# Kernel tuning notes

Hardware: AMD Instinct MI355X
Metric: run time of the kernel (lower is better)

## Reference

```python
import jax, jax.numpy as jnp
import numpy as np

B_GRAPHS, N_NODES = 16, 4096
IN_CH, HID = 256, 512
HEADS, HC = 1, 512  # SGFormerAttention(hidden, heads=1, head_channels=hidden)
NUM_LAYERS = 2
LN_EPS = 1e-5
QK_EPS = 1e-6


def setup_inputs() -> dict:
    key = jax.random.key(0)
    ks = jax.random.split(key, 10)

    def w(k, shape, scale=0.02):
        return jax.random.normal(k, shape, jnp.float32) * scale

    inp = {
        "x": jax.random.normal(ks[0], (B_GRAPHS * N_NODES, IN_CH), jnp.float32),
        "fc0_w": w(ks[1], (HID, IN_CH)),
        "fc0_b": jnp.zeros((HID,), jnp.float32),
        "ln0_g": jnp.ones((HID,), jnp.float32),
        "ln0_b": jnp.zeros((HID,), jnp.float32),
        "q0_w": w(ks[2], (HEADS * HC, HID)),
        "k0_w": w(ks[3], (HEADS * HC, HID)),
        "v0_w": w(ks[4], (HEADS * HC, HID)),
        "ln1_g": jnp.ones((HID,), jnp.float32),
        "ln1_b": jnp.zeros((HID,), jnp.float32),
        "q1_w": w(ks[5], (HEADS * HC, HID)),
        "k1_w": w(ks[6], (HEADS * HC, HID)),
        "v1_w": w(ks[7], (HEADS * HC, HID)),
        "ln2_g": jnp.ones((HID,), jnp.float32),
        "ln2_b": jnp.zeros((HID,), jnp.float32),
        "batch": jnp.repeat(jnp.arange(B_GRAPHS, dtype=jnp.int32), N_NODES),
        "num_graphs": B_GRAPHS,
    }
    return inp


def layernorm(x, g, b):
    mu = x.mean(axis=-1, keepdims=True)
    var = ((x - mu) ** 2).mean(axis=-1, keepdims=True)
    return (x - mu) / jnp.sqrt(var + LN_EPS) * g + b


def sg_attention(x, qw, kw, vw):
    # x: [B, N, HID]; linear (kernelized) global attention, softmax-free.
    B, N, _ = x.shape
    q = (x @ qw.T).reshape(B, N, HEADS, HC)
    k = (x @ kw.T).reshape(B, N, HEADS, HC)
    v = (x @ vw.T).reshape(B, N, HEADS, HC)
    q = jnp.where(q == 0, QK_EPS, q)
    k = jnp.where(k == 0, QK_EPS, k)
    q = q / jnp.linalg.norm(q, axis=-1, keepdims=True)
    k = k / jnp.linalg.norm(k, axis=-1, keepdims=True)
    kvs = jnp.einsum('blhm,blhd->bhmd', k, v)          # [B,H,HC,HC]
    num = jnp.einsum('bnhm,bhmd->bnhd', q, kvs) + N * v
    ks_sum = k.sum(axis=1)                             # [B,H,HC]
    denom = jnp.einsum('bnhm,bhm->bnh', q, ks_sum)[..., None] + float(N)
    return (num / denom).mean(axis=2)                  # [B,N,HC] (mean over heads)


def reference(x, fc0_w, fc0_b, ln0_g, ln0_b,
              q0_w, k0_w, v0_w, ln1_g, ln1_b,
              q1_w, k1_w, v1_w, ln2_g, ln2_b,
              batch, num_graphs):
    total = x.shape[0]
    # stable sort by graph id, remember inverse permutation
    indices = jnp.argsort(batch, stable=True)
    rev_perm = jnp.zeros((total,), jnp.int32).at[indices].set(
        jnp.arange(total, dtype=jnp.int32))
    xs = x[indices]
    # uniform graph sizes -> to_dense_batch is a reshape; mask is all-True
    h = xs.reshape(num_graphs, total // num_graphs, x.shape[1])
    h = h @ fc0_w.T + fc0_b
    h = jax.nn.relu(layernorm(h, ln0_g, ln0_b))  # dropout inactive (eval)
    layers = [h]
    for (qw, kw, vw, g, b) in ((q0_w, k0_w, v0_w, ln1_g, ln1_b),
                               (q1_w, k1_w, v1_w, ln2_g, ln2_b)):
        a = sg_attention(layers[-1], qw, kw, vw)
        a = (a + layers[-1]) / 2.0
        a = jax.nn.relu(layernorm(a, g, b))
        layers.append(a)
    out = layers[-1].reshape(total, -1)
    return out[rev_perm]
```

## Files before the change

### kernel.cpp

```cpp
#include <hip/hip_runtime.h>

#define TNODES 65536
#define NGRAPH 16
#define NNODE  4096
#define INCH   256
#define HID    512

using u16 = unsigned short;
using u32 = unsigned int;
using v8s = __attribute__((ext_vector_type(8))) short;
using v4f = __attribute__((ext_vector_type(4))) float;

__device__ __forceinline__ float bf2f(u16 u) {
    union { u32 i; float f; } v; v.i = ((u32)u) << 16; return v.f;
}
__device__ __forceinline__ u16 f2bf(float f) {
    union { float f; u32 i; } v; v.f = f;
    u32 x = v.i;
    return (u16)((x + 0x7fffu + ((x >> 16) & 1u)) >> 16);
}
__device__ __forceinline__ void up4(uint2 p, float* f) {
    f[0] = __uint_as_float(p.x << 16); f[1] = __uint_as_float(p.x & 0xffff0000u);
    f[2] = __uint_as_float(p.y << 16); f[3] = __uint_as_float(p.y & 0xffff0000u);
}
__device__ __forceinline__ uint2 pk4(float a, float b, float c, float d) {
    uint2 r;
    r.x = (u32)f2bf(a) | ((u32)f2bf(b) << 16);
    r.y = (u32)f2bf(c) | ((u32)f2bf(d) << 16);
    return r;
}

#define MFMA(a, b, c) __builtin_amdgcn_mfma_f32_16x16x32_bf16((a), (b), (c), 0, 0, 0)

#define GLD16(gp, sp) __builtin_amdgcn_global_load_lds( \
    (const __attribute__((address_space(1))) u32*)(const void*)(gp), \
    (__attribute__((address_space(3))) u32*)(void*)(sp), 16, 0, 0)

__global__ void k_cvt4(const float* __restrict__ s, u16* __restrict__ d, int n4) {
    for (int i = blockIdx.x * blockDim.x + threadIdx.x; i < n4; i += gridDim.x * blockDim.x) {
        float4 f = ((const float4*)s)[i];
        ((uint2*)d)[i] = pk4(f.x, f.y, f.z, f.w);
    }
}

__global__ void k_zero(float* __restrict__ p, int n) {
    int i = blockIdx.x * 256 + threadIdx.x;
    if (i < n) p[i] = 0.f;
}

__global__ void k_red4(const u16* __restrict__ p, u16* __restrict__ o, int n8) {
    const size_t P = (size_t)NGRAPH * HID * HID;
    for (int i = blockIdx.x * blockDim.x + threadIdx.x; i < n8; i += gridDim.x * blockDim.x) {
        size_t b = (size_t)i * 8;
        float s[8] = {0.f, 0.f, 0.f, 0.f, 0.f, 0.f, 0.f, 0.f};
        #pragma unroll
        for (int ss = 0; ss < 4; ++ss) {
            v8s v = *(const v8s*)(p + ss * P + b);
            const u16* vp = (const u16*)&v;
            #pragma unroll
            for (int j = 0; j < 8; ++j) s[j] += bf2f(vp[j]);
        }
        uint2 lo = pk4(s[0], s[1], s[2], s[3]);
        uint2 hi = pk4(s[4], s[5], s[6], s[7]);
        uint4 w; w.x = lo.x; w.y = lo.y; w.z = hi.x; w.w = hi.y;
        *(uint4*)(o + b) = w;
    }
}

template<int LDK, int KLEN>
__device__ __forceinline__ void gemm_core(const u16* __restrict__ A,
                                          const u16* __restrict__ W,
                                          u16* sA, u16* sW, v4f (&acc)[8][2]) {
    const int t = threadIdx.x, lane = t & 63;
    const int q = lane >> 4, m15 = lane & 15;
    const int w = t >> 6, wr = w >> 2, wc = w & 3;

    #pragma unroll
    for (int n = 0; n < 8; ++n)
        #pragma unroll
        for (int rt = 0; rt < 2; ++rt)
            #pragma unroll
            for (int e = 0; e < 4; ++e) acc[n][rt][e] = 0.f;

    int aoff[2], woff[8];
    #pragma unroll
    for (int rt = 0; rt < 2; ++rt) {
        int r = wr * 32 + rt * 16 + m15;
        aoff[rt] = r * 32 + ((q ^ ((r >> 1) & 3)) * 8);
    }
    #pragma unroll
    for (int n = 0; n < 8; ++n) {
        int r = wc * 128 + n * 16 + m15;
        woff[n] = r * 32 + ((q ^ ((r >> 1) & 3)) * 8);
    }

    auto stage = [&](int k0, int buf) {
        u16* dW = sW + buf * (512 * 32);
        #pragma unroll
        for (int p = 0; p < 4; ++p) {
            int sf = p * 512 + t, row = sf >> 2, sl = sf & 3;
            int gc = k0 + ((sl ^ ((row >> 1) & 3)) * 8);
            GLD16(W + (size_t)row * LDK + gc, dW + sf * 8);
        }
        if (t < 256) {
            int row = t >> 2, sl = t & 3;
            int gc = k0 + ((sl ^ ((row >> 1) & 3)) * 8);
            GLD16(A + (size_t)row * LDK + gc, sA + buf * (64 * 32) + t * 8);
        }
    };

    stage(0, 0);
    __syncthreads();
    const int KT = KLEN / 32;
    int cur = 0;
    for (int kt = 0; kt < KT; ++kt) {
        if (kt + 1 < KT) stage((kt + 1) * 32, cur ^ 1);
        const u16* cA = sA + cur * (64 * 32);
        const u16* cW = sW + cur * (512 * 32);
        v8s b0 = *(const v8s*)(cA + aoff[0]);
        v8s b1 = *(const v8s*)(cA + aoff[1]);
        #pragma unroll
        for (int n = 0; n < 8; ++n) {
            v8s af = *(const v8s*)(cW + woff[n]);
            acc[n][0] = MFMA(af, b0, acc[n][0]);
            acc[n][1] = MFMA(af, b1, acc[n][1]);
        }
        __syncthreads();
        cur ^= 1;
    }
}


__launch_bounds__(512, 4)
__global__ void k_fc(const u16* __restrict__ xb, const u16* __restrict__ wb,
                     const float* __restrict__ bias, const float* __restrict__ lg,
                     const float* __restrict__ lb, u16* __restrict__ h) {
    __shared__ u16 sA[2][64 * 32];
    __shared__ u16 sW[2][512 * 32];
    __shared__ float red[2][64][4];
    __shared__ float rowv[2][64];
    const int t = threadIdx.x, lane = t & 63, w = t >> 6;
    const int q = lane >> 4, m15 = lane & 15;
    const int wr = w >> 2, wc = w & 3;
    const int bx = (int)blockIdx.x;
    const int swz = (bx & 7) * ((int)gridDim.x >> 3) + (bx >> 3);
    const int r0 = swz * 64;
    v4f acc[8][2];
    gemm_core<INCH, INCH>(xb + (size_t)r0 * INCH, wb, &sA[0][0], &sW[0][0], acc);

    float sm0 = 0.f, sm1 = 0.f, sq0 = 0.f, sq1 = 0.f;
    #pragma unroll
    for (int n = 0; n < 8; ++n) {
        int c = wc * 128 + n * 16 + q * 4;
        float4 bi = *(const float4*)(bias + c);
        const float* bp = &bi.x;
        #pragma unroll
        for (int rt = 0; rt < 2; ++rt)
            #pragma unroll
            for (int e = 0; e < 4; ++e) {
                float a = acc[n][rt][e] + bp[e];
                acc[n][rt][e] = a;
                if (rt == 0) { sm0 += a; sq0 += a * a; } else { sm1 += a; sq1 += a * a; }
            }
    }
    sm0 += __shfl_xor(sm0, 16); sm0 += __shfl_xor(sm0, 32);
    sq0 += __shfl_xor(sq0, 16); sq0 += __shfl_xor(sq0, 32);
    sm1 += __shfl_xor(sm1, 16); sm1 += __shfl_xor(sm1, 32);
    sq1 += __shfl_xor(sq1, 16); sq1 += __shfl_xor(sq1, 32);
    if (lane < 16) {
        red[0][wr * 32 + m15][wc] = sm0; red[0][wr * 32 + 16 + m15][wc] = sm1;
        red[1][wr * 32 + m15][wc] = sq0; red[1][wr * 32 + 16 + m15][wc] = sq1;
    }
    __syncthreads();
    if (t < 64) {
        float tt = red[0][t][0] + red[0][t][1] + red[0][t][2] + red[0][t][3];
        float t2 = red[1][t][0] + red[1][t][1] + red[1][t][2] + red[1][t][3];
        float mu = tt * (1.f / HID);
        float rs = rsqrtf(t2 * (1.f / HID) - mu * mu + 1e-5f);
        rowv[0][t] = mu; rowv[1][t] = rs;
    }
    __syncthreads();
    #pragma unroll
    for (int n = 0; n < 8; ++n) {
        int c = wc * 128 + n * 16 + q * 4;
        float4 g4 = *(const float4*)(lg + c);
        float4 b4 = *(const float4*)(lb + c);
        #pragma unroll
        for (int rt = 0; rt < 2; ++rt) {
            int row = wr * 32 + rt * 16 + m15;
            float mu = rowv[0][row], rs = rowv[1][row];
            float v0 = (acc[n][rt][0] - mu) * rs * g4.x + b4.x;
            float v1 = (acc[n][rt][1] - mu) * rs * g4.y + b4.y;
            float v2 = (acc[n][rt][2] - mu) * rs * g4.z + b4.z;
            float v3 = (acc[n][rt][3] - mu) * rs * g4.w + b4.w;
            v0 = v0 > 0.f ? v0 : 0.f; v1 = v1 > 0.f ? v1 : 0.f;
            v2 = v2 > 0.f ? v2 : 0.f; v3 = v3 > 0.f ? v3 : 0.f;
            *(uint2*)&h[(size_t)(r0 + row) * HID + c] = pk4(v0, v1, v2, v3);
        }
    }
}

__launch_bounds__(512, 4)
__global__ void k_proj(const u16* __restrict__ hsrc, const u16* __restrict__ wkb,
                       const u16* __restrict__ wvb, u16* __restrict__ kt,
                       u16* __restrict__ vt, float* __restrict__ vo,
                       float* __restrict__ ksum) {
    __shared__ char smem[8192 + 65536 + 1024 + 256];
    u16* sA = (u16*)smem;
    u16* sW = (u16*)(smem + 8192);
    u16* sT = sW;
    float (*red)[4] = (float(*)[4])(smem + 8192 + 65536);
    float* rowv = (float*)(smem + 8192 + 65536 + 1024);
    const int t = threadIdx.x, lane = t & 63, w = t >> 6;
    const int q = lane >> 4, m15 = lane & 15;
    const int wr = w >> 2, wc = w & 3;
    const int bx = (int)blockIdx.x;
    const int swz = (bx & 7) * ((int)gridDim.x >> 3) + (bx >> 3);
    const int r0 = swz * 64;
    const int g = swz >> 6;
    const int lbase = (swz & 63) * 64;
    const int mode = blockIdx.y;
    v4f acc[8][2];
    gemm_core<HID, HID>(hsrc + (size_t)r0 * HID, mode ? wvb : wkb,
                        sA, sW, acc);

    if (mode == 0) {
        float sq0 = 0.f, sq1 = 0.f;
        #pragma unroll
        for (int n = 0; n < 8; ++n)
            #pragma unroll
            for (int rt = 0; rt < 2; ++rt)
                #pragma unroll
                for (int e = 0; e < 4; ++e) {
                    float vv = acc[n][rt][e];
                    if (vv == 0.f) vv = 1e-6f;
                    acc[n][rt][e] = vv;
                    if (rt == 0) sq0 += vv * vv; else sq1 += vv * vv;
                }
        sq0 += __shfl_xor(sq0, 16); sq0 += __shfl_xor(sq0, 32);
        sq1 += __shfl_xor(sq1, 16); sq1 += __shfl_xor(sq1, 32);
        if (lane < 16) {
            red[wr * 32 + m15][wc] = sq0; red[wr * 32 + 16 + m15][wc] = sq1;
        }
        __syncthreads();
        if (t < 64)
            rowv[t] = rsqrtf(red[t][0] + red[t][1] + red[t][2] + red[t][3]);
        __syncthreads();
        #pragma unroll
        for (int n = 0; n < 8; ++n)
            #pragma unroll
            for (int rt = 0; rt < 2; ++rt) {
                int row = wr * 32 + rt * 16 + m15;
                float rn = rowv[row];
                #pragma unroll
                for (int e = 0; e < 4; ++e) {
                    int c = wc * 128 + n * 16 + q * 4 + e;
                    sT[(c << 6) + (row ^ ((c & 7) << 3))] = f2bf(acc[n][rt][e] * rn);
                }
            }
        __syncthreads();
        const int ch = t;
        u16* op = kt + ((size_t)(g * 512 + ch)) * NNODE + lbase;
        float sum = 0.f;
        #pragma unroll
        for (int jj = 0; jj < 8; ++jj) {
            v8s cvec = *(const v8s*)&sT[(ch << 6) + jj * 8];
            int l0 = (jj ^ (ch & 7)) * 8;
            *(v8s*)(op + l0) = cvec;
            const u16* cp = (const u16*)&cvec;
            #pragma unroll
            for (int i = 0; i < 8; ++i) sum += bf2f(cp[i]);
        }
        atomicAdd(&ksum[g * 512 + ch], sum);
    } else {
        #pragma unroll
        for (int n = 0; n < 8; ++n) {
            int c = wc * 128 + n * 16 + q * 4;
            #pragma unroll
            for (int rt = 0; rt < 2; ++rt) {
                int row = wr * 32 + rt * 16 + m15;
                float4 o = {acc[n][rt][0], acc[n][rt][1], acc[n][rt][2], acc[n][rt][3]};
                *(float4*)&vo[(size_t)(r0 + row) * HID + c] = o;
                #pragma unroll
                for (int e = 0; e < 4; ++e)
                    sT[((c + e) << 6) + (row ^ (((c + e) & 7) << 3))] = f2bf(acc[n][rt][e]);
            }
        }
        __syncthreads();
        const int ch = t;
        u16* op = vt + ((size_t)(g * 512 + ch)) * NNODE + lbase;
        #pragma unroll
        for (int jj = 0; jj < 8; ++jj) {
            v8s cvec = *(const v8s*)&sT[(ch << 6) + jj * 8];
            int l0 = (jj ^ (ch & 7)) * 8;
            *(v8s*)(op + l0) = cvec;
        }
    }
}

__launch_bounds__(512, 4)
__global__ void k_kvmm2(const u16* __restrict__ kt, const u16* __restrict__ vt,
                        u16* __restrict__ kvp) {
    __shared__ u16 sA[2][64 * 32];
    __shared__ u16 sW[2][512 * 32];
    const int t = threadIdx.x, lane = t & 63, w = t >> 6;
    const int q = lane >> 4, m15 = lane & 15;
    const int wr = w >> 2, wc = w & 3;
    const int bx = (int)blockIdx.x;
    const int swz = (bx & 7) * 64 + (bx >> 3);
    const int db = swz & 7, s = (swz >> 3) & 3, g = swz >> 5;
    const u16* A = vt + ((size_t)(g * 512 + db * 64)) * NNODE + s * 1024;
    const u16* W = kt + ((size_t)(g * 512)) * NNODE + s * 1024;
    v4f acc[8][2];
    gemm_core<NNODE, 1024>(A, W, &sA[0][0], &sW[0][0], acc);
    u16* plane = kvp + (size_t)s * NGRAPH * HID * HID;
    #pragma unroll
    for (int n = 0; n < 8; ++n) {
        int m = wc * 128 + n * 16 + q * 4;
        #pragma unroll
        for (int rt = 0; rt < 2; ++rt) {
            int d = db * 64 + wr * 32 + rt * 16 + m15;
            *(uint2*)&plane[((size_t)(g * 512) + d) * 512 + m] =
                pk4(acc[n][rt][0], acc[n][rt][1], acc[n][rt][2], acc[n][rt][3]);
        }
    }
}

__launch_bounds__(512, 4)
__global__ void k_qnorm(const u16* __restrict__ hsrc, const u16* __restrict__ qwb,
                        const float* __restrict__ ks, u16* __restrict__ qo,
                        float* __restrict__ dnv) {
    __shared__ u16 sA[2][64 * 32];
    __shared__ u16 sW[2][512 * 32];
    __shared__ float red[2][64][4];
    __shared__ float rowv[64];
    const int t = threadIdx.x, lane = t & 63, w = t >> 6;
    const int q = lane >> 4, m15 = lane & 15;
    const int wr = w >> 2, wc = w & 3;
    const int bx = (int)blockIdx.x;
    const int swz = (bx & 7) * ((int)gridDim.x >> 3) + (bx >> 3);
    const int r0 = swz * 64;
    const int gi = swz >> 6;
    v4f acc[8][2];
    gemm_core<HID, HID>(hsrc + (size_t)r0 * HID, qwb, &sA[0][0], &sW[0][0], acc);

    float ss0 = 0.f, ss1 = 0.f, ws0 = 0.f, ws1 = 0.f;
    #pragma unroll
    for (int n = 0; n < 8; ++n) {
        int c = wc * 128 + n * 16 + q * 4;
        float4 kv = *(const float4*)(ks + (gi << 9) + c);
        const float* kp = &kv.x;
        #pragma unroll
        for (int rt = 0; rt < 2; ++rt)
            #pragma unroll
            for (int e = 0; e < 4; ++e) {
                float vv = acc[n][rt][e];
                if (vv == 0.f) vv = 1e-6f;
                acc[n][rt][e] = vv;
                if (rt == 0) { ss0 += vv * vv; ws0 += vv * kp[e]; }
                else         { ss1 += vv * vv; ws1 += vv * kp[e]; }
            }
    }
    ss0 += __shfl_xor(ss0, 16); ss0 += __shfl_xor(ss0, 32);
    ss1 += __shfl_xor(ss1, 16); ss1 += __shfl_xor(ss1, 32);
    ws0 += __shfl_xor(ws0, 16); ws0 += __shfl_xor(ws0, 32);
    ws1 += __shfl_xor(ws1, 16); ws1 += __shfl_xor(ws1, 32);
    if (lane < 16) {
        red[0][wr * 32 + m15][wc] = ss0; red[0][wr * 32 + 16 + m15][wc] = ss1;
        red[1][wr * 32 + m15][wc] = ws0; red[1][wr * 32 + 16 + m15][wc] = ws1;
    }
    __syncthreads();
    if (t < 64) {
        float st = red[0][t][0] + red[0][t][1] + red[0][t][2] + red[0][t][3];
        float wt = red[1][t][0] + red[1][t][1] + red[1][t][2] + red[1][t][3];
        float rn = rsqrtf(st);
        rowv[t] = rn;
        dnv[r0 + t] = 1.f / (rn * wt + (float)NNODE);
    }
    __syncthreads();
    #pragma unroll
    for (int n = 0; n < 8; ++n) {
        int c = wc * 128 + n * 16 + q * 4;
        #pragma unroll
        for (int rt = 0; rt < 2; ++rt) {
            int row = wr * 32 + rt * 16 + m15;
            float rn = rowv[row];
            *(uint2*)&qo[(size_t)(r0 + row) * HID + c] =
                pk4(acc[n][rt][0] * rn, acc[n][rt][1] * rn,
                    acc[n][rt][2] * rn, acc[n][rt][3] * rn);
        }
    }
}

__launch_bounds__(512, 4)
__global__ void k_attn2(const u16* __restrict__ qhat, const u16* __restrict__ kvstb,
                        const float* __restrict__ dnv, const float* __restrict__ vsrc,
                        const u16* __restrict__ hsrc, const float* __restrict__ lg,
                        const float* __restrict__ lb, u16* __restrict__ outb,
                        float* __restrict__ outf) {
    __shared__ u16 sA[2][64 * 32];
    __shared__ u16 sW[2][512 * 32];
    __shared__ float red[2][64][4];
    __shared__ float rowv[2][64];
    const int t = threadIdx.x, lane = t & 63, w = t >> 6;
    const int q = lane >> 4, m15 = lane & 15;
    const int wr = w >> 2, wc = w & 3;
    const int bx = (int)blockIdx.x;
    const int swz = (bx & 7) * ((int)gridDim.x >> 3) + (bx >> 3);
    const int r0 = swz * 64;
    const int gi = swz >> 6;
    v4f acc[8][2];
    gemm_core<HID, HID>(qhat + (size_t)r0 * HID, kvstb + (size_t)gi * HID * HID,
                        &sA[0][0], &sW[0][0], acc);

    const float dv0 = dnv[r0 + wr * 32 + m15];
    const float dv1 = dnv[r0 + wr * 32 + 16 + m15];
    float sm0 = 0.f, sm1 = 0.f, sq0 = 0.f, sq1 = 0.f;
    #pragma unroll
    for (int n = 0; n < 8; ++n) {
        int c = wc * 128 + n * 16 + q * 4;
        #pragma unroll
        for (int rt = 0; rt < 2; ++rt) {
            int row = wr * 32 + rt * 16 + m15;
            size_t og = (size_t)(r0 + row) * HID + c;
            float hh[4]; up4(*(const uint2*)&hsrc[og], hh);
            float4 vv = *(const float4*)&vsrc[og];
            const float* vp = &vv.x;
            float dv = rt ? dv1 : dv0;
            #pragma unroll
            for (int e = 0; e < 4; ++e) {
                float a = ((acc[n][rt][e] + (float)NNODE * vp[e]) * dv + hh[e]) * 0.5f;
                acc[n][rt][e] = a;
                if (rt == 0) { sm0 += a; sq0 += a * a; } else { sm1 += a; sq1 += a * a; }
            }
        }
    }
    sm0 += __shfl_xor(sm0, 16); sm0 += __shfl_xor(sm0, 32);
    sq0 += __shfl_xor(sq0, 16); sq0 += __shfl_xor(sq0, 32);
    sm1 += __shfl_xor(sm1, 16); sm1 += __shfl_xor(sm1, 32);
    sq1 += __shfl_xor(sq1, 16); sq1 += __shfl_xor(sq1, 32);
    if (lane < 16) {
        red[0][wr * 32 + m15][wc] = sm0; red[0][wr * 32 + 16 + m15][wc] = sm1;
        red[1][wr * 32 + m15][wc] = sq0; red[1][wr * 32 + 16 + m15][wc] = sq1;
    }
    __syncthreads();
    if (t < 64) {
        float tt = red[0][t][0] + red[0][t][1] + red[0][t][2] + red[0][t][3];
        float t2 = red[1][t][0] + red[1][t][1] + red[1][t][2] + red[1][t][3];
        float mu = tt * (1.f / HID);
        float rs = rsqrtf(t2 * (1.f / HID) - mu * mu + 1e-5f);
        rowv[0][t] = mu; rowv[1][t] = rs;
    }
    __syncthreads();
    #pragma unroll
    for (int n = 0; n < 8; ++n) {
        int c = wc * 128 + n * 16 + q * 4;
        float4 g4 = *(const float4*)(lg + c);
        float4 b4 = *(const float4*)(lb + c);
        #pragma unroll
        for (int rt = 0; rt < 2; ++rt) {
            int row = wr * 32 + rt * 16 + m15;
            float mu = rowv[0][row], rs = rowv[1][row];
            float v0 = (acc[n][rt][0] - mu) * rs * g4.x + b4.x;
            float v1 = (acc[n][rt][1] - mu) * rs * g4.y + b4.y;
            float v2 = (acc[n][rt][2] - mu) * rs * g4.z + b4.z;
            float v3 = (acc[n][rt][3] - mu) * rs * g4.w + b4.w;
            v0 = v0 > 0.f ? v0 : 0.f; v1 = v1 > 0.f ? v1 : 0.f;
            v2 = v2 > 0.f ? v2 : 0.f; v3 = v3 > 0.f ? v3 : 0.f;
            size_t og = (size_t)(r0 + row) * HID + c;
            if (outf) {
                float4 o = {v0, v1, v2, v3};
                *(float4*)&outf[og] = o;
            } else {
                *(uint2*)&outb[og] = pk4(v0, v1, v2, v3);
            }
        }
    }
}

extern "C" void kernel_launch(void* const* d_in, const int* in_sizes, int n_in,
                              void* d_out, int out_size, void* d_ws, size_t ws_size,
                              hipStream_t stream) {
    const float* x    = (const float*)d_in[0];
    const float* fc0w = (const float*)d_in[1];
    const float* fc0b = (const float*)d_in[2];
    const float* ln0g = (const float*)d_in[3];
    const float* ln0b = (const float*)d_in[4];
    const float* q0w  = (const float*)d_in[5];
    const float* k0w  = (const float*)d_in[6];
    const float* v0w  = (const float*)d_in[7];
    const float* ln1g = (const float*)d_in[8];
    const float* ln1b = (const float*)d_in[9];
    const float* q1w  = (const float*)d_in[10];
    const float* k1w  = (const float*)d_in[11];
    const float* v1w  = (const float*)d_in[12];
    const float* ln2g = (const float*)d_in[13];
    const float* ln2b = (const float*)d_in[14];

    const size_t M64 = (size_t)TNODES * HID * 2;
    const size_t PL  = (size_t)NGRAPH * HID * HID * 2;
    char* wsc = (char*)d_ws;
    u16*   H   = (u16*)wsc;
    u16*   Kt  = (u16*)(wsc + M64);
    u16*   Vt  = (u16*)(wsc + 2 * M64);
    u16*   KVp = (u16*)(wsc + 3 * M64);
    u16*   KVb = (u16*)(wsc + 3 * M64 + 4 * PL);
    float* KS  = (float*)(wsc + 3 * M64 + 5 * PL);
    float* DNV = KS + NGRAPH * HID;
    u16*   Wc  = (u16*)((char*)DNV + (size_t)TNODES * sizeof(float));
    u16* fc0wb = Wc;
    u16* q0b = Wc + 131072;
    u16* k0b = Wc + 393216;
    u16* v0b = Wc + 655360;
    u16* q1b = Wc + 917504;
    u16* k1b = Wc + 1179648;
    u16* v1b = Wc + 1441792;
    u16* Xb  = Vt;
    u16* QH  = Vt;
    float* V = (float*)d_out;

    dim3 b256(256), b512(512);
    k_cvt4<<<dim3(64),  b256, 0, stream>>>(fc0w, fc0wb, HID * INCH / 4);
    k_cvt4<<<dim3(64),  b256, 0, stream>>>(q0w, q0b, HID * HID / 4);
    k_cvt4<<<dim3(64),  b256, 0, stream>>>(k0w, k0b, HID * HID / 4);
    k_cvt4<<<dim3(64),  b256, 0, stream>>>(v0w, v0b, HID * HID / 4);
    k_cvt4<<<dim3(64),  b256, 0, stream>>>(q1w, q1b, HID * HID / 4);
    k_cvt4<<<dim3(64),  b256, 0, stream>>>(k1w, k1b, HID * HID / 4);
    k_cvt4<<<dim3(64),  b256, 0, stream>>>(v1w, v1b, HID * HID / 4);
    k_cvt4<<<dim3(1024), b256, 0, stream>>>(x, Xb, TNODES * INCH / 4);

    k_fc<<<dim3(TNODES / 64), b512, 0, stream>>>(Xb, fc0wb, fc0b, ln0g, ln0b, H);

    k_zero<<<dim3(32), b256, 0, stream>>>(KS, NGRAPH * HID);
    k_proj<<<dim3(TNODES / 64, 2), b512, 0, stream>>>(H, k0b, v0b, Kt, Vt, V, KS);
    k_kvmm2<<<dim3(512), b512, 0, stream>>>(Kt, Vt, KVp);
    k_red4<<<dim3(2048), b256, 0, stream>>>(KVp, KVb, NGRAPH * HID * HID / 8);
    k_qnorm<<<dim3(TNODES / 64), b512, 0, stream>>>(H, q0b, KS, QH, DNV);
    k_attn2<<<dim3(TNODES / 64), b512, 0, stream>>>(QH, KVb, DNV, V, H, ln1g, ln1b,
                                                    H, nullptr);

    k_zero<<<dim3(32), b256, 0, stream>>>(KS, NGRAPH * HID);
    k_proj<<<dim3(TNODES / 64, 2), b512, 0, stream>>>(H, k1b, v1b, Kt, Vt, V, KS);
    k_kvmm2<<<dim3(512), b512, 0, stream>>>(Kt, Vt, KVp);
    k_red4<<<dim3(2048), b256, 0, stream>>>(KVp, KVb, NGRAPH * HID * HID / 8);
    k_qnorm<<<dim3(TNODES / 64), b512, 0, stream>>>(H, q1b, KS, QH, DNV);
    k_attn2<<<dim3(TNODES / 64), b512, 0, stream>>>(QH, KVb, DNV, V, H, ln2g, ln2b,
                                                    nullptr, (float*)d_out);
}
```

Baseline: 1.094 ms.

## Deepen GEMM staging to two tiles ahead and rework transpose LDS swizzle

The shared GEMM core now issues global-to-LDS loads two k-tiles ahead instead of one. Each wait uses an explicit s_waitcnt vmcnt count plus a raw s_barrier, where before a full __syncthreads followed each tile. The goal is to keep more memory traffic in flight behind the MFMA work. Separately, the XOR swizzle used when transposing K/V tiles through LDS is changed to a different pattern, aiming to cut bank conflicts on the scattered bf16 writes. The hand-counted vmcnt values depend on the exact number of loads per thread and could break correctness if the compiler reorders or adds memory ops.

```diff
diff --git a/kernel.cpp b/kernel.cpp
--- a/kernel.cpp
+++ b/kernel.cpp
@@ -35,6 +35,8 @@
 #define GLD16(gp, sp) __builtin_amdgcn_global_load_lds( \
     (const __attribute__((address_space(1))) u32*)(const void*)(gp), \
     (__attribute__((address_space(3))) u32*)(void*)(sp), 16, 0, 0)
+
+#define CFENCE() asm volatile("" ::: "memory")
 
 __global__ void k_cvt4(const float* __restrict__ s, u16* __restrict__ d, int n4) {
     for (int i = blockIdx.x * blockDim.x + threadIdx.x; i < n4; i += gridDim.x * blockDim.x) {
@@ -109,12 +111,21 @@
         }
     };
 
+    const int KT = KLEN / 32;
     stage(0, 0);
-    __syncthreads();
-    const int KT = KLEN / 32;
+    stage(32, 1);
     int cur = 0;
+    const bool lowt = (t < 256);
     for (int kt = 0; kt < KT; ++kt) {
-        if (kt + 1 < KT) stage((kt + 1) * 32, cur ^ 1);
+        if (kt + 1 < KT) {
+            if (lowt) asm volatile("s_waitcnt vmcnt(5)" ::: "memory");
+            else      asm volatile("s_waitcnt vmcnt(4)" ::: "memory");
+        } else {
+            asm volatile("s_waitcnt vmcnt(0)" ::: "memory");
+        }
+        __builtin_amdgcn_s_barrier();
+        CFENCE();
+        __builtin_amdgcn_sched_barrier(0);
         const u16* cA = sA + cur * (64 * 32);
         const u16* cW = sW + cur * (512 * 32);
         v8s b0 = *(const v8s*)(cA + aoff[0]);
@@ -125,11 +136,18 @@
             acc[n][0] = MFMA(af, b0, acc[n][0]);
             acc[n][1] = MFMA(af, b1, acc[n][1]);
         }
-        __syncthreads();
+        CFENCE();
+        __builtin_amdgcn_s_barrier();
+        CFENCE();
+        if (kt + 2 < KT) stage((kt + 2) * 32, cur);
         cur ^= 1;
     }
 }
 
+
+__device__ __forceinline__ int tswz(int c) {
+    return (((c >> 2) & 3) << 4) ^ ((c & 3) << 3);
+}
 
 __launch_bounds__(512, 4)
 __global__ void k_fc(const u16* __restrict__ xb, const u16* __restrict__ wb,
@@ -255,17 +273,18 @@
                 #pragma unroll
                 for (int e = 0; e < 4; ++e) {
                     int c = wc * 128 + n * 16 + q * 4 + e;
-                    sT[(c << 6) + (row ^ ((c & 7) << 3))] = f2bf(acc[n][rt][e] * rn);
+                    sT[(c << 6) + (row ^ tswz(c))] = f2bf(acc[n][rt][e] * rn);
                 }
             }
         __syncthreads();
         const int ch = t;
+        const int xs = (((ch >> 2) & 3) << 1) ^ (ch & 3);
         u16* op = kt + ((size_t)(g * 512 + ch)) * NNODE + lbase;
         float sum = 0.f;
         #pragma unroll
         for (int jj = 0; jj < 8; ++jj) {
             v8s cvec = *(const v8s*)&sT[(ch << 6) + jj * 8];
-            int l0 = (jj ^ (ch & 7)) * 8;
+            int l0 = (jj ^ xs) * 8;
             *(v8s*)(op + l0) = cvec;
             const u16* cp = (const u16*)&cvec;
             #pragma unroll
@@ -283,16 +302,17 @@
                 *(float4*)&vo[(size_t)(r0 + row) * HID + c] = o;
                 #pragma unroll
                 for (int e = 0; e < 4; ++e)
-                    sT[((c + e) << 6) + (row ^ (((c + e) & 7) << 3))] = f2bf(acc[n][rt][e]);
+                    sT[((c + e) << 6) + (row ^ tswz(c + e))] = f2bf(acc[n][rt][e]);
             }
         }
         __syncthreads();
         const int ch = t;
+        const int xs = (((ch >> 2) & 3) << 1) ^ (ch & 3);
         u16* op = vt + ((size_t)(g * 512 + ch)) * NNODE + lbase;
         #pragma unroll
         for (int jj = 0; jj < 8; ++jj) {
             v8s cvec = *(const v8s*)&sT[(ch << 6) + jj * 8];
-            int l0 = (jj ^ (ch & 7)) * 8;
+            int l0 = (jj ^ xs) * 8;
             *(v8s*)(op + l0) = cvec;
         }
     }
```

After: 1.095 ms. Within noise of the previous version (+0.1%).
